# Kernel optimization log

Hardware: AMD Instinct MI355X
Metric: run time of the kernel (lower is better)

Reference implementation:

```python
import jax, jax.numpy as jnp
import numpy as np

B, S = 4, 1024
IN_F, OUT_F = 8192, 8192
ACT_BITS = 8


def setup_inputs() -> dict:
    key = jax.random.key(0)
    k1, k2, k3, k4 = jax.random.split(key, 4)
    x = jax.random.normal(k1, (B, S, IN_F), dtype=jnp.float32)
    # each int8 byte packs two 4-bit exponent nibbles; stored as int32 values in [0, 256)
    packed_exponents = jax.random.randint(k2, (OUT_F, IN_F // 2), 0, 256, dtype=jnp.int32)
    # signs are +/-1 per weight element
    signs = jax.random.randint(k3, (OUT_F, IN_F), 0, 2, dtype=jnp.int32) * 2 - 1
    bias = jax.random.normal(k4, (OUT_F,), dtype=jnp.float32)
    activation_scale = jnp.float32(0.02)  # delta_lsb for int8 activation quant
    min_exp = -14  # python int constant (buffer min_exp in the torch module)
    return {
        "x": x,
        "packed_exponents": packed_exponents,
        "signs": signs,
        "bias": bias,
        "activation_scale": activation_scale,
        "min_exp": min_exp,
    }


def reference(x, packed_exponents, signs, bias, activation_scale, min_exp):
    q_max = 2 ** (ACT_BITS - 1) - 1   # 127
    q_min = -2 ** (ACT_BITS - 1)      # -128
    orig_shape = x.shape
    x2 = x.reshape(-1, orig_shape[-1])  # [N, IN_F]

    # int8 activation quantization (kept in float; values are exact small ints)
    a_quant = jnp.clip(jnp.round(x2 / activation_scale), q_min, q_max)

    # unpack two 4-bit exponent nibbles per byte: low nibble first, then high
    lo = packed_exponents & 0xF
    hi = (packed_exponents >> 4) & 0xF
    exps = jnp.stack([lo, hi], axis=-1).reshape(OUT_F, IN_F)  # [OUT_F, IN_F]

    # dequantized log-domain weights: sign * 2^(nibble + min_exp)
    w = signs.astype(jnp.float32) * jnp.exp2((exps + min_exp).astype(jnp.float32))

    # batched matvec (the CUDA kernel does one row of this per launch) + dequant + bias
    out = (a_quant @ w.T) * activation_scale + bias  # [N, OUT_F]
    return out.reshape(*orig_shape[:-1], OUT_F)
```

## Files before the change

kernel.cpp:

```cpp
#include <hip/hip_runtime.h>
#include <hip/hip_bf16.h>
#include <stdint.h>

#define N_TOK 4096
#define KF    8192
#define NF    8192

#define BM 256
#define BN 256

typedef __attribute__((ext_vector_type(8))) short short8;
typedef __attribute__((ext_vector_type(4))) float f32x4;

#define GLOBAL_P(p) ((const __attribute__((address_space(1))) void*)(p))
#define LDS_P(p)    ((__attribute__((address_space(3))) void*)(p))

__global__ void quant_x(const float* __restrict__ x, const float* __restrict__ scale_p,
                        uint16_t* __restrict__ a) {
    const float s = *scale_p;
    const int n8 = N_TOK * KF / 8;
    const int stride = gridDim.x * blockDim.x;
    for (int i = blockIdx.x * blockDim.x + threadIdx.x; i < n8; i += stride) {
        const float4* xp = (const float4*)(x + (size_t)i * 8);
        float4 v0 = xp[0], v1 = xp[1];
        float q[8] = {v0.x, v0.y, v0.z, v0.w, v1.x, v1.y, v1.z, v1.w};
        union { uint16_t u16[8]; short8 v; } o;
        #pragma unroll
        for (int j = 0; j < 8; ++j) {
            float t = rintf(q[j] / s);
            t = fminf(fmaxf(t, -128.f), 127.f);
            union { float f; uint32_t u; } cv; cv.f = t;
            o.u16[j] = (uint16_t)(cv.u >> 16);
        }
        *(short8*)(a + (size_t)i * 8) = o.v;
    }
}

__global__ void dequant_w(const int* __restrict__ packed, const int* __restrict__ signs,
                          const int* __restrict__ minexp_p, uint16_t* __restrict__ w) {
    const int me = *minexp_p;
    const int ebase = (me + 127) << 7;
    const int n4 = NF * (KF / 2) / 4;
    const int stride = gridDim.x * blockDim.x;
    for (int i = blockIdx.x * blockDim.x + threadIdx.x; i < n4; i += stride) {
        int4 p  = ((const int4*)packed)[i];
        int4 s0 = ((const int4*)signs)[(size_t)i * 2];
        int4 s1 = ((const int4*)signs)[(size_t)i * 2 + 1];
        int pw[4] = {p.x, p.y, p.z, p.w};
        int sg[8] = {s0.x, s0.y, s0.z, s0.w, s1.x, s1.y, s1.z, s1.w};
        union { uint16_t u16[8]; short8 v; } o;
        #pragma unroll
        for (int j = 0; j < 4; ++j) {
            int lo = pw[j] & 0xF, hi = (pw[j] >> 4) & 0xF;
            o.u16[2 * j]     = (uint16_t)((ebase + (lo << 7)) | (sg[2 * j]     < 0 ? 0x8000 : 0));
            o.u16[2 * j + 1] = (uint16_t)((ebase + (hi << 7)) | (sg[2 * j + 1] < 0 ? 0x8000 : 0));
        }
        *(short8*)(w + (size_t)i * 8) = o.v;
    }
}

#define BARRIER()  __builtin_amdgcn_s_barrier()
#define SCHED0()   __builtin_amdgcn_sched_barrier(0)
#define WAITVM4()  do { asm volatile("s_waitcnt vmcnt(4)"); SCHED0(); } while (0)
#define WAITVM0()  do { asm volatile("s_waitcnt vmcnt(0)"); SCHED0(); } while (0)
#define SP1 __builtin_amdgcn_s_setprio(1)
#define SP0 __builtin_amdgcn_s_setprio(0)

__global__ __launch_bounds__(512, 2) void gemm_bt(
        const uint16_t* __restrict__ A, const uint16_t* __restrict__ W,
        const float* __restrict__ bias, const float* __restrict__ scale_p,
        float* __restrict__ out) {
    __shared__ uint16_t ldsA[4 * 256 * 32];
    __shared__ uint16_t ldsB[4 * 256 * 32];

    const int tid  = threadIdx.x;
    const int wid  = tid >> 6, lane = tid & 63;
    const int wr = wid >> 2, wc = wid & 3;
    const int rlane = lane & 15, kgrp = lane >> 4;

    const int bid = blockIdx.x;
    const int xcd = bid & 7;
    const int i_l = bid >> 3;
    const int gen = i_l >> 5;
    const int il  = i_l & 31;
    const int by  = gen * 8 + (il >> 2);
    const int bx  = xcd * 4 + (il & 3);
    const int rowA0 = by * BM;
    const int colB0 = bx * BN;

    const int o0 = tid * 16, o1 = (512 + tid) * 16;
    const int l0 = o0 ^ (((o0 >> 9) & 1) << 5);
    const int l1 = o1 ^ (((o1 >> 9) & 1) << 5);
    const char* gA0 = (const char*)A + ((size_t)(rowA0 + (l0 >> 6)) * KF) * 2 + (l0 & 63);
    const char* gA1 = (const char*)A + ((size_t)(rowA0 + (l1 >> 6)) * KF) * 2 + (l1 & 63);
    const char* gB0 = (const char*)W + ((size_t)(colB0 + (l0 >> 6)) * KF) * 2 + (l0 & 63);
    const char* gB1 = (const char*)W + ((size_t)(colB0 + (l1 >> 6)) * KF) * 2 + (l1 & 63);
    const int ldst0 = wid * 1024;
    const int ldst1 = 8192 + wid * 1024;

    int aoff[8], boff[4];
    #pragma unroll
    for (int i = 0; i < 8; ++i) {
        int row = wr * 128 + i * 16 + rlane;
        int o = row * 64 + kgrp * 16;
        aoff[i] = o ^ (((o >> 9) & 1) << 5);
    }
    #pragma unroll
    for (int n = 0; n < 4; ++n) {
        int row = wc * 64 + n * 16 + rlane;
        int o = row * 64 + kgrp * 16;
        boff[n] = o ^ (((o >> 9) & 1) << 5);
    }

#define STAGE_A(j) do { \
    char* b_ = (char*)ldsA + ((j) & 3) * 16384; \
    __builtin_amdgcn_global_load_lds(GLOBAL_P(gA0 + (size_t)(j) * 64), LDS_P(b_ + ldst0), 16, 0, 0); \
    __builtin_amdgcn_global_load_lds(GLOBAL_P(gA1 + (size_t)(j) * 64), LDS_P(b_ + ldst1), 16, 0, 0); \
} while (0)
#define STAGE_B(j) do { \
    char* b_ = (char*)ldsB + ((j) & 3) * 16384; \
    __builtin_amdgcn_global_load_lds(GLOBAL_P(gB0 + (size_t)(j) * 64), LDS_P(b_ + ldst0), 16, 0, 0); \
    __builtin_amdgcn_global_load_lds(GLOBAL_P(gB1 + (size_t)(j) * 64), LDS_P(b_ + ldst1), 16, 0, 0); \
} while (0)
#define LDAH(DST, H, SLOT) do { \
    const char* p_ = (const char*)ldsA + (SLOT) * 16384; \
    _Pragma("unroll") for (int i_ = 0; i_ < 4; ++i_) \
        DST[i_] = *(const short8*)(p_ + aoff[(H) * 4 + i_]); \
} while (0)
#define LDB4(DST, SLOT) do { \
    const char* p_ = (const char*)ldsB + (SLOT) * 16384; \
    _Pragma("unroll") for (int i_ = 0; i_ < 4; ++i_) \
        DST[i_] = *(const short8*)(p_ + boff[i_]); \
} while (0)
#define MFMAH(H, A4, B4) do { \
    SP1; \
    _Pragma("unroll") for (int mm_ = 0; mm_ < 4; ++mm_) \
        _Pragma("unroll") for (int nn_ = 0; nn_ < 4; ++nn_) \
            acc[(H) * 4 + mm_][nn_] = __builtin_amdgcn_mfma_f32_16x16x32_bf16( \
                A4[mm_], B4[nn_], acc[(H) * 4 + mm_][nn_], 0, 0, 0); \
    SP0; \
} while (0)

#define WINDOW(BC, BN_, SC, SN, JST, VM) do { \
    BARRIER(); \
    LDAH(aQ, 1, SC);             \
    STAGE_A(JST); \
    MFMAH(0, aP, BC); \
    LDAH(aP, 0, SN);             \
    LDB4(BN_, SN);               \
    STAGE_B(JST); \
    MFMAH(1, aQ, BC); \
    VM; \
} while (0)
#define WINDOW_NS(BC, BN_, SC, SN, VM) do { \
    BARRIER(); \
    LDAH(aQ, 1, SC); \
    MFMAH(0, aP, BC); \
    LDAH(aP, 0, SN); \
    LDB4(BN_, SN); \
    MFMAH(1, aQ, BC); \
    VM; \
} while (0)

    f32x4 acc[8][4] = {};
    short8 aP[4], aQ[4], bP[4], bQ[4];

    STAGE_A(0); STAGE_B(0);
    STAGE_A(1); STAGE_B(1);
    STAGE_A(2); STAGE_B(2);
    WAITVM4();
    BARRIER();
    LDAH(aP, 0, 0);
    LDB4(bP, 0);

    for (int kt = 0; kt < 63; ++kt) {
        const int j0 = 4 * kt;
        WINDOW(bP, bQ, 0, 1, j0 + 3, WAITVM4());
        WINDOW(bQ, bP, 1, 2, j0 + 4, WAITVM4());
        WINDOW(bP, bQ, 2, 3, j0 + 5, WAITVM4());
        WINDOW(bQ, bP, 3, 0, j0 + 6, WAITVM4());
    }

    WINDOW(bP, bQ, 0, 1, 255, WAITVM4());
    WINDOW_NS(bQ, bP, 1, 2, WAITVM0());
    WINDOW_NS(bP, bQ, 2, 3, (void)0);
    BARRIER();
    LDAH(aQ, 1, 3);
    MFMAH(0, aP, bQ);
    MFMAH(1, aQ, bQ);

    const float s = *scale_p;
    const int colbase = colB0 + wc * 64 + rlane;
    const int rowbase = rowA0 + wr * 128 + kgrp * 4;
    #pragma unroll
    for (int n = 0; n < 4; ++n) {
        const float bv = bias[colbase + n * 16];
        #pragma unroll
        for (int mf = 0; mf < 8; ++mf) {
            #pragma unroll
            for (int r = 0; r < 4; ++r)
                out[(size_t)(rowbase + mf * 16 + r) * NF + colbase + n * 16] = acc[mf][n][r] * s + bv;
        }
    }
#undef STAGE_A
#undef STAGE_B
#undef LDAH
#undef LDB4
#undef MFMAH
#undef WINDOW
#undef WINDOW_NS
}

extern "C" void kernel_launch(void* const* d_in, const int* in_sizes, int n_in,
                              void* d_out, int out_size, void* d_ws, size_t ws_size,
                              hipStream_t stream) {
    const float* x      = (const float*)d_in[0];
    const int*   packed = (const int*)d_in[1];
    const int*   signs  = (const int*)d_in[2];
    const float* bias   = (const float*)d_in[3];
    const float* scale  = (const float*)d_in[4];
    const int*   minexp = (const int*)d_in[5];
    float* out = (float*)d_out;

    uint16_t* A = (uint16_t*)d_ws;
    uint16_t* W = (uint16_t*)((char*)d_ws + (size_t)N_TOK * KF * 2);

    quant_x<<<2048, 256, 0, stream>>>(x, scale, A);
    dequant_w<<<2048, 256, 0, stream>>>(packed, signs, minexp, W);
    gemm_bt<<<(N_TOK / BM) * (NF / BN), 512, 0, stream>>>(A, W, bias, scale, out);
}
```

Measured before the change: 604.2 us.

## Merge quant and dequant kernels into one launch; simplify B register ping-pong

```diff
diff --git a/kernel.cpp b/kernel.cpp
--- a/kernel.cpp
+++ b/kernel.cpp
@@ -15,12 +15,16 @@
 #define GLOBAL_P(p) ((const __attribute__((address_space(1))) void*)(p))
 #define LDS_P(p)    ((__attribute__((address_space(3))) void*)(p))
 
-__global__ void quant_x(const float* __restrict__ x, const float* __restrict__ scale_p,
-                        uint16_t* __restrict__ a) {
+__global__ void prep(const float* __restrict__ x, const float* __restrict__ scale_p,
+                     uint16_t* __restrict__ a,
+                     const int* __restrict__ packed, const int* __restrict__ signs,
+                     const int* __restrict__ minexp_p, uint16_t* __restrict__ w) {
     const float s = *scale_p;
+    const int stride = gridDim.x * blockDim.x;
+    const int tid0 = blockIdx.x * blockDim.x + threadIdx.x;
+
     const int n8 = N_TOK * KF / 8;
-    const int stride = gridDim.x * blockDim.x;
-    for (int i = blockIdx.x * blockDim.x + threadIdx.x; i < n8; i += stride) {
+    for (int i = tid0; i < n8; i += stride) {
         const float4* xp = (const float4*)(x + (size_t)i * 8);
         float4 v0 = xp[0], v1 = xp[1];
         float q[8] = {v0.x, v0.y, v0.z, v0.w, v1.x, v1.y, v1.z, v1.w};
@@ -34,15 +38,11 @@
         }
         *(short8*)(a + (size_t)i * 8) = o.v;
     }
-}
-
-__global__ void dequant_w(const int* __restrict__ packed, const int* __restrict__ signs,
-                          const int* __restrict__ minexp_p, uint16_t* __restrict__ w) {
+
     const int me = *minexp_p;
     const int ebase = (me + 127) << 7;
     const int n4 = NF * (KF / 2) / 4;
-    const int stride = gridDim.x * blockDim.x;
-    for (int i = blockIdx.x * blockDim.x + threadIdx.x; i < n4; i += stride) {
+    for (int i = tid0; i < n4; i += stride) {
         int4 p  = ((const int4*)packed)[i];
         int4 s0 = ((const int4*)signs)[(size_t)i * 2];
         int4 s1 = ((const int4*)signs)[(size_t)i * 2 + 1];
@@ -141,24 +141,17 @@
     SP0; \
 } while (0)
 
-#define WINDOW(BC, BN_, SC, SN, JST, VM) do { \
+#define WINDOW(SC, SN, JST, VM) do { \
     BARRIER(); \
     LDAH(aQ, 1, SC);             \
     STAGE_A(JST); \
-    MFMAH(0, aP, BC); \
+    MFMAH(0, aP, bP); \
     LDAH(aP, 0, SN);             \
-    LDB4(BN_, SN);               \
+    LDB4(bQ, SN);                \
     STAGE_B(JST); \
-    MFMAH(1, aQ, BC); \
-    VM; \
-} while (0)
-#define WINDOW_NS(BC, BN_, SC, SN, VM) do { \
-    BARRIER(); \
-    LDAH(aQ, 1, SC); \
-    MFMAH(0, aP, BC); \
-    LDAH(aP, 0, SN); \
-    LDB4(BN_, SN); \
-    MFMAH(1, aQ, BC); \
+    MFMAH(1, aQ, bP); \
+    { short8 t0 = bQ[0], t1 = bQ[1], t2 = bQ[2], t3 = bQ[3]; \
+      bP[0] = t0; bP[1] = t1; bP[2] = t2; bP[3] = t3; } \
     VM; \
 } while (0)
 
@@ -175,19 +168,30 @@
 
     for (int kt = 0; kt < 63; ++kt) {
         const int j0 = 4 * kt;
-        WINDOW(bP, bQ, 0, 1, j0 + 3, WAITVM4());
-        WINDOW(bQ, bP, 1, 2, j0 + 4, WAITVM4());
-        WINDOW(bP, bQ, 2, 3, j0 + 5, WAITVM4());
-        WINDOW(bQ, bP, 3, 0, j0 + 6, WAITVM4());
-    }
-
-    WINDOW(bP, bQ, 0, 1, 255, WAITVM4());
-    WINDOW_NS(bQ, bP, 1, 2, WAITVM0());
-    WINDOW_NS(bP, bQ, 2, 3, (void)0);
+        WINDOW(0, 1, j0 + 3, WAITVM4());
+        WINDOW(1, 2, j0 + 4, WAITVM4());
+        WINDOW(2, 3, j0 + 5, WAITVM4());
+        WINDOW(3, 0, j0 + 6, WAITVM4());
+    }
+
+    WINDOW(0, 1, 255, WAITVM4());
+    BARRIER();
+    LDAH(aQ, 1, 1);
+    MFMAH(0, aP, bP);
+    LDAH(aP, 0, 2); LDB4(bQ, 2);
+    MFMAH(1, aQ, bP);
+    bP[0] = bQ[0]; bP[1] = bQ[1]; bP[2] = bQ[2]; bP[3] = bQ[3];
+    WAITVM0();
+    BARRIER();
+    LDAH(aQ, 1, 2);
+    MFMAH(0, aP, bP);
+    LDAH(aP, 0, 3); LDB4(bQ, 3);
+    MFMAH(1, aQ, bP);
+    bP[0] = bQ[0]; bP[1] = bQ[1]; bP[2] = bQ[2]; bP[3] = bQ[3];
     BARRIER();
     LDAH(aQ, 1, 3);
-    MFMAH(0, aP, bQ);
-    MFMAH(1, aQ, bQ);
+    MFMAH(0, aP, bP);
+    MFMAH(1, aQ, bP);
 
     const float s = *scale_p;
     const int colbase = colB0 + wc * 64 + rlane;
@@ -208,7 +212,6 @@
 #undef LDB4
 #undef MFMAH
 #undef WINDOW
-#undef WINDOW_NS
 }
 
 extern "C" void kernel_launch(void* const* d_in, const int* in_sizes, int n_in,
@@ -225,7 +228,6 @@
     uint16_t* A = (uint16_t*)d_ws;
     uint16_t* W = (uint16_t*)((char*)d_ws + (size_t)N_TOK * KF * 2);
 
-    quant_x<<<2048, 256, 0, stream>>>(x, scale, A);
-    dequant_w<<<2048, 256, 0, stream>>>(packed, signs, minexp, W);
+    prep<<<2048, 256, 0, stream>>>(x, scale, A, packed, signs, minexp, W);
     gemm_bt<<<(N_TOK / BM) * (NF / BN), 512, 0, stream>>>(A, W, bias, scale, out);
 }
```

Result: no change. 608.5 us (+0.7%).
